# Optimization experiments

Measured on AMD Instinct MI355X. Metric: run time of the kernel, lower is better.

Reference implementation:

```python
import jax, jax.numpy as jnp
import numpy as np

DT = 1.0 / 60.0  # physics timestep
NUM_BODY = 20

# ---- quaternion helpers (xyzw convention, matching the repo) ----

def quat_from_rotvec(rv):
    # rv: [..., 3] axis-angle -> quaternion [..., 4] (x,y,z,w)
    angle = jnp.linalg.norm(rv, axis=-1, keepdims=True)
    half = 0.5 * angle
    safe = jnp.where(angle < 1e-8, 1.0, angle)
    s = jnp.where(angle < 1e-8, 0.5 - angle * angle / 48.0, jnp.sin(half) / safe)
    return jnp.concatenate([rv * s, jnp.cos(half)], axis=-1)


def flip_quat_by_w(q):
    return jnp.where(q[..., 3:4] < 0, -q, q)


def quat_to_vec6d(q):
    # first two columns of the rotation matrix, row-major flattened -> [..., 6]
    x, y, z, w = q[..., 0], q[..., 1], q[..., 2], q[..., 3]
    r00 = 1 - 2 * (y * y + z * z)
    r10 = 2 * (x * y + z * w)
    r20 = 2 * (x * z - y * w)
    r01 = 2 * (x * y - z * w)
    r11 = 1 - 2 * (x * x + z * z)
    r21 = 2 * (y * z + x * w)
    return jnp.stack([r00, r01, r10, r11, r20, r21], axis=-1)


def quat_apply(q, v):
    # rotate v [..., 3] by quaternion q [..., 4]; broadcasts over leading dims
    xyz, w = q[..., :3], q[..., 3:4]
    t = 2.0 * jnp.cross(xyz, v)
    return v + w * t + jnp.cross(xyz, t)


def quat_multiply(p, q):
    pv, pw = p[..., :3], p[..., 3:4]
    qv, qw = q[..., :3], q[..., 3:4]
    v = pw * qv + qw * pv + jnp.cross(pv, qv)
    w = pw * qw - jnp.sum(pv * qv, axis=-1, keepdims=True)
    return jnp.concatenate([v, w], axis=-1)


def quat_integrate(q, omega, dt):
    # q_{t+1} = normalize(q + 0.5*dt * (omega_quat * q))
    omega_q = jnp.concatenate([omega, jnp.zeros_like(omega[..., :1])], axis=-1)
    dq = quat_multiply(omega_q, q)
    r = q + 0.5 * dt * dq
    return r / jnp.linalg.norm(r, axis=-1, keepdims=True)


def integrate_state(state, delta, dt):
    # state: [B, NB, 13] = pos(3) | rot quat(4) | vel(3) | avel(3)
    B, NB, _ = state.shape
    pos, rot = state[..., 0:3], state[..., 3:7]
    vel, avel = state[..., 7:10], state[..., 10:13]
    root_rot = state[:, 0:1, 3:7]                       # [B, 1, 4]
    d3 = delta.reshape(B, -1, 3)                        # [B, 2*NB, 3]
    true_d = quat_apply(root_rot, d3).reshape(B, NB, 6)
    lin, ang = true_d[..., :3], true_d[..., 3:]
    next_vel = vel + lin
    next_avel = avel + ang
    next_pos = pos + next_vel * dt
    next_rot = quat_integrate(rot, next_avel, dt)
    return jnp.concatenate([next_pos, next_rot, next_vel, next_avel], axis=-1)


def setup_inputs() -> dict:
    key = jax.random.key(0)
    ks = jax.random.split(key, 12)
    B = 32768
    inp = {
        "state": jax.random.normal(ks[0], (B, NUM_BODY, 13), jnp.float32),
        "action": jax.random.normal(ks[1], (B, 57), jnp.float32),
        "n_observation": jax.random.normal(ks[2], (B, 300), jnp.float32),
        "W1": jax.random.normal(ks[3], (414, 512), jnp.float32) * 0.05,
        "b1": jax.random.normal(ks[4], (512,), jnp.float32) * 0.05,
        "W2": jax.random.normal(ks[5], (512, 512), jnp.float32) * 0.05,
        "b2": jax.random.normal(ks[6], (512,), jnp.float32) * 0.05,
        "W3": jax.random.normal(ks[7], (512, 120), jnp.float32) * 0.05,
        "b3": jax.random.normal(ks[8], (120,), jnp.float32) * 0.05,
        "delta_mean": jax.random.normal(ks[9], (120,), jnp.float32) * 0.01,
        "delta_std": jax.random.uniform(ks[10], (120,), jnp.float32) + 0.5,
    }
    return inp


def reference(state, action, n_observation, W1, b1, W2, b2, W3, b3, delta_mean, delta_std):
    B = action.shape[0]
    # action rotvecs -> quats -> 6d representation
    aq = flip_quat_by_w(quat_from_rotvec(action.reshape(-1, 3)))
    a6 = quat_to_vec6d(aq).reshape(B, -1)               # [B, 114]
    x = jnp.concatenate([n_observation, a6], axis=-1)   # [B, 414]
    h = jax.nn.relu(x @ W1 + b1)
    h = jax.nn.relu(h @ W2 + b2)
    n_delta = h @ W3 + b3                                # [B, 120]
    delta = n_delta * delta_std + delta_mean             # unnormalize
    return integrate_state(state, delta, DT)
```

## Files before the change

kernel.cpp:

```cpp
#include <hip/hip_runtime.h>
#include <hip/hip_bf16.h>
#include <math.h>

#define DT (1.0f / 60.0f)

typedef __bf16 bf16x8 __attribute__((ext_vector_type(8)));
typedef float f32x4 __attribute__((ext_vector_type(4)));

#define XSTRIDE 848
#define HSTRIDE 1040

struct __attribute__((packed)) f4u {
    float x, y, z, w;
};

__global__ __launch_bounds__(256) void prep_weights(
    const float* __restrict__ W1, const float* __restrict__ W2,
    const float* __restrict__ W3, __hip_bfloat16* __restrict__ W1p,
    __hip_bfloat16* __restrict__ W2p, __hip_bfloat16* __restrict__ W3p) {
    int idx = blockIdx.x * 256 + threadIdx.x;
    if (idx < 212992) {
        int d = idx;
        int e = d & 7, l = (d >> 3) & 63, t = d >> 9;
        int nt = t & 31, ks = t >> 5;
        int n = nt * 16 + (l & 15);
        int k = ks * 32 + (l >> 4) * 8 + e;
        W1p[d] = __float2bfloat16(k < 414 ? W1[k * 512 + n] : 0.0f);
        return;
    }
    idx -= 212992;
    if (idx < 262144) {
        int d = idx;
        int e = d & 7, l = (d >> 3) & 63, t = d >> 9;
        int nt = t & 31, ks = t >> 5;
        int n = nt * 16 + (l & 15);
        int k = ks * 32 + (l >> 4) * 8 + e;
        W2p[d] = __float2bfloat16(W2[k * 512 + n]);
        return;
    }
    idx -= 262144;
    if (idx < 65536) {
        int d = idx;
        int e = d & 7, l = (d >> 3) & 63, t = d >> 9;
        int nt = t & 7, ks = t >> 3;
        int n = nt * 16 + (l & 15);
        int k = ks * 32 + (l >> 4) * 8 + e;
        W3p[d] = __float2bfloat16(n < 120 ? W3[k * 120 + n] : 0.0f);
    }
}

template <int KSTEPS, int NT, int JF, int ASTRIDE>
__device__ __forceinline__ void mlp_layer(const char* Abase, const char* Bbase,
                                          int laneOff, f32x4 (&acc)[4][JF],
                                          bf16x8 (&wpre)[JF]) {
    bf16x8 w0[JF], w1[JF];
#pragma unroll
    for (int j = 0; j < JF; j++) w0[j] = wpre[j];
#pragma unroll 2
    for (int ks = 0; ks < KSTEPS; ks++) {
        if (ks + 1 < KSTEPS) {
            if ((ks & 1) == 0) {
#pragma unroll
                for (int j = 0; j < JF; j++)
                    w1[j] = *(const bf16x8*)(Bbase + (((ks + 1) * NT + j) << 10) + laneOff);
            } else {
#pragma unroll
                for (int j = 0; j < JF; j++)
                    w0[j] = *(const bf16x8*)(Bbase + (((ks + 1) * NT + j) << 10) + laneOff);
            }
        }
        bf16x8 ax[4];
#pragma unroll
        for (int i = 0; i < 4; i++)
            ax[i] = *(const bf16x8*)(Abase + ks * 64 + i * 16 * ASTRIDE);
#pragma unroll
        for (int i = 0; i < 4; i++)
#pragma unroll
            for (int j = 0; j < JF; j++)
                acc[i][j] = __builtin_amdgcn_mfma_f32_16x16x32_bf16(
                    (ks & 1) ? w1[j] : w0[j], ax[i], acc[i][j], 0, 0, 0);
    }
}

__device__ __forceinline__ void store_h_relu_t(const f32x4 (&acc)[4][4],
                                               char* smem, const float* bias,
                                               int wn, int lrow, int kgrp) {
#pragma unroll
    for (int j = 0; j < 4; j++) {
        int f = wn * 64 + j * 16 + kgrp * 4;
        float4 bb = *(const float4*)(bias + f);
#pragma unroll
        for (int i = 0; i < 4; i++) {
            float v0 = acc[i][j][0] + bb.x;
            float v1 = acc[i][j][1] + bb.y;
            float v2 = acc[i][j][2] + bb.z;
            float v3 = acc[i][j][3] + bb.w;
            v0 = v0 > 0.0f ? v0 : 0.0f;
            v1 = v1 > 0.0f ? v1 : 0.0f;
            v2 = v2 > 0.0f ? v2 : 0.0f;
            v3 = v3 > 0.0f ? v3 : 0.0f;
            union { __hip_bfloat162 h2[2]; uint2 u; } pk;
            pk.h2[0] = __float22bfloat162_rn(make_float2(v0, v1));
            pk.h2[1] = __float22bfloat162_rn(make_float2(v2, v3));
            *(uint2*)(smem + (i * 16 + lrow) * HSTRIDE + f * 2) = pk.u;
        }
    }
}

__device__ __forceinline__ void quat_apply3(float qx, float qy, float qz,
                                            float qw, float vx, float vy,
                                            float vz, float& ox, float& oy,
                                            float& oz) {
    float tx = 2.0f * (qy * vz - qz * vy);
    float ty = 2.0f * (qz * vx - qx * vz);
    float tz = 2.0f * (qx * vy - qy * vx);
    ox = vx + qw * tx + (qy * tz - qz * ty);
    oy = vy + qw * ty + (qz * tx - qx * tz);
    oz = vz + qw * tz + (qx * ty - qy * tx);
}

__global__ __launch_bounds__(512, 4) void fused_mlp(
    const float* __restrict__ obs, const float* __restrict__ action,
    const __hip_bfloat16* __restrict__ W1p, const float* __restrict__ b1,
    const __hip_bfloat16* __restrict__ W2p, const float* __restrict__ b2,
    const __hip_bfloat16* __restrict__ W3p, const float* __restrict__ b3,
    const float* __restrict__ dstd, const float* __restrict__ dmean,
    const float* __restrict__ state, float* __restrict__ out) {
    alignas(16) __shared__ char smem[64 * HSTRIDE];
    const int tid = threadIdx.x;
    const int blk = blockIdx.x;
    const int lane = tid & 63, wn = tid >> 6;
    const int lrow = lane & 15, kgrp = lane >> 4;
    const int laneOff = lane * 16;

    bf16x8 wpre[4];
#pragma unroll
    for (int j = 0; j < 4; j++)
        wpre[j] = *(const bf16x8*)((const char*)W1p + (wn << 12) + (j << 10) + laneOff);

    {
        const float4* og = (const float4*)obs + (size_t)blk * 64 * 75;
#pragma unroll
        for (int i = 0; i < 10; i++) {
            int f = tid + i * 512;
            if (f < 4800) {
                int row = f / 75;
                int c4 = f - row * 75;
                float4 v = og[f];
                union { __hip_bfloat162 h2[2]; uint2 u; } pk;
                pk.h2[0] = __float22bfloat162_rn(make_float2(v.x, v.y));
                pk.h2[1] = __float22bfloat162_rn(make_float2(v.z, v.w));
                *(uint2*)(smem + row * XSTRIDE + c4 * 8) = pk.u;
            }
        }
#pragma unroll
        for (int i = 0; i < 3; i++) {
            int q = tid + i * 512;
            if (q < 1216) {
                int row = q / 19;
                int j = q - row * 19;
                const float* a = action + ((size_t)(blk * 64 + row)) * 57 + j * 3;
                float rx = a[0], ry = a[1], rz = a[2];
                float ang = sqrtf(rx * rx + ry * ry + rz * rz);
                float half = 0.5f * ang;
                float s;
                if (ang < 1e-8f)
                    s = 0.5f - ang * ang * (1.0f / 48.0f);
                else
                    s = __sinf(half) / ang;
                float qx = rx * s, qy = ry * s, qz = rz * s, qw = __cosf(half);
                union { __hip_bfloat16 h[6]; uint u[3]; } pq;
                pq.h[0] = __float2bfloat16(1.0f - 2.0f * (qy * qy + qz * qz));
                pq.h[1] = __float2bfloat16(2.0f * (qx * qy - qz * qw));
                pq.h[2] = __float2bfloat16(2.0f * (qx * qy + qz * qw));
                pq.h[3] = __float2bfloat16(1.0f - 2.0f * (qx * qx + qz * qz));
                pq.h[4] = __float2bfloat16(2.0f * (qx * qz - qy * qw));
                pq.h[5] = __float2bfloat16(2.0f * (qy * qz + qx * qw));
                char* p = smem + row * XSTRIDE + 600 + j * 12;
                *(uint*)p = pq.u[0];
                *(uint*)(p + 4) = pq.u[1];
                *(uint*)(p + 8) = pq.u[2];
            }
        }
        if (tid < 320) {
            int row = tid / 5;
            int p = tid - row * 5;
            *(uint*)(smem + row * XSTRIDE + 828 + p * 4) = 0u;
        }
    }
    __syncthreads();

    f32x4 acc[4][4];
    f32x4 zero4 = {0.0f, 0.0f, 0.0f, 0.0f};
#pragma unroll
    for (int i = 0; i < 4; i++)
#pragma unroll
        for (int j = 0; j < 4; j++) acc[i][j] = zero4;

    mlp_layer<13, 32, 4, XSTRIDE>(smem + lrow * XSTRIDE + kgrp * 16,
                                  (const char*)W1p + (wn << 12), laneOff, acc,
                                  wpre);
#pragma unroll
    for (int j = 0; j < 4; j++)
        wpre[j] = *(const bf16x8*)((const char*)W2p + (wn << 12) + (j << 10) + laneOff);
    __syncthreads();
    store_h_relu_t(acc, smem, b1, wn, lrow, kgrp);
    __syncthreads();

#pragma unroll
    for (int i = 0; i < 4; i++)
#pragma unroll
        for (int j = 0; j < 4; j++) acc[i][j] = zero4;
    mlp_layer<16, 32, 4, HSTRIDE>(smem + lrow * HSTRIDE + kgrp * 16,
                                  (const char*)W2p + (wn << 12), laneOff, acc,
                                  wpre);
    const char* Bb3 = (const char*)W3p + (wn << 10);
    bf16x8 c0 = *(const bf16x8*)(Bb3 + laneOff);
    __syncthreads();
    store_h_relu_t(acc, smem, b2, wn, lrow, kgrp);
    __syncthreads();

    f32x4 a3[4];
#pragma unroll
    for (int i = 0; i < 4; i++) a3[i] = zero4;
    {
        const char* Ab = smem + lrow * HSTRIDE + kgrp * 16;
        bf16x8 c1;
#pragma unroll 2
        for (int ks = 0; ks < 16; ks++) {
            if (ks + 1 < 16) {
                if ((ks & 1) == 0)
                    c1 = *(const bf16x8*)(Bb3 + ((ks + 1) << 13) + laneOff);
                else
                    c0 = *(const bf16x8*)(Bb3 + ((ks + 1) << 13) + laneOff);
            }
            bf16x8 ax[4];
#pragma unroll
            for (int i = 0; i < 4; i++)
                ax[i] = *(const bf16x8*)(Ab + ks * 64 + i * 16 * HSTRIDE);
#pragma unroll
            for (int i = 0; i < 4; i++)
                a3[i] = __builtin_amdgcn_mfma_f32_16x16x32_bf16(
                    (ks & 1) ? c1 : c0, ax[i], a3[i], 0, 0, 0);
        }
    }
    __syncthreads();

    float* dl = (float*)smem;
    {
        int f = wn * 16 + kgrp * 4;
        if (f < 120) {
            float4 bb = *(const float4*)(b3 + f);
            float4 sc = *(const float4*)(dstd + f);
            float4 mn = *(const float4*)(dmean + f);
            int bo0 = (f + 0) / 6, o0 = bo0 * 13 + (f + 0) - bo0 * 6;
            int bo1 = (f + 1) / 6, o1 = bo1 * 13 + (f + 1) - bo1 * 6;
            int bo2 = (f + 2) / 6, o2 = bo2 * 13 + (f + 2) - bo2 * 6;
            int bo3 = (f + 3) / 6, o3 = bo3 * 13 + (f + 3) - bo3 * 6;
#pragma unroll
            for (int i = 0; i < 4; i++) {
                float* rs = dl + (i * 16 + lrow) * 260;
                rs[o0] = (a3[i][0] + bb.x) * sc.x + mn.x;
                rs[o1] = (a3[i][1] + bb.y) * sc.y + mn.y;
                rs[o2] = (a3[i][2] + bb.z) * sc.z + mn.z;
                rs[o3] = (a3[i][3] + bb.w) * sc.w + mn.w;
            }
        }
    }
    __syncthreads();

#pragma unroll
    for (int it = 0; it < 3; it++) {
        int idx = tid + it * 512;
        if (idx < 1280) {
            int lr = idx / 20;
            int body = idx - lr * 20;
            const float* sb = state + ((size_t)(blk * 64 + lr)) * 260 + body * 13;
            f4u s0 = *(const f4u*)sb;
            f4u s1 = *(const f4u*)(sb + 4);
            f4u s2 = *(const f4u*)(sb + 8);
            float s12 = sb[12];
            f4u rq = *(const f4u*)(state + ((size_t)(blk * 64 + lr)) * 260 + 3);

            float* slot = dl + lr * 260 + body * 13;
            float d0 = slot[0], d1 = slot[1], d2 = slot[2];
            float d3 = slot[3], d4 = slot[4], d5 = slot[5];

            float lx, ly, lz, ax, ay, az;
            quat_apply3(rq.x, rq.y, rq.z, rq.w, d0, d1, d2, lx, ly, lz);
            quat_apply3(rq.x, rq.y, rq.z, rq.w, d3, d4, d5, ax, ay, az);

            float vx = s1.w + lx, vy = s2.x + ly, vz = s2.y + lz;
            float wx = s2.z + ax, wy = s2.w + ay, wz = s12 + az;
            float px = s0.x + vx * DT, py = s0.y + vy * DT, pz = s0.z + vz * DT;

            float rx = s0.w, ry = s1.x, rz = s1.y, rw = s1.z;
            float dqx = rw * wx + (wy * rz - wz * ry);
            float dqy = rw * wy + (wz * rx - wx * rz);
            float dqz = rw * wz + (wx * ry - wy * rx);
            float dqw = -(wx * rx + wy * ry + wz * rz);
            float h = 0.5f * DT;
            float nx = rx + h * dqx, ny = ry + h * dqy, nz = rz + h * dqz,
                  nw = rw + h * dqw;
            float inv = 1.0f / sqrtf(nx * nx + ny * ny + nz * nz + nw * nw);

            slot[0] = px;
            slot[1] = py;
            slot[2] = pz;
            slot[3] = nx * inv;
            slot[4] = ny * inv;
            slot[5] = nz * inv;
            slot[6] = nw * inv;
            slot[7] = vx;
            slot[8] = vy;
            slot[9] = vz;
            slot[10] = wx;
            slot[11] = wy;
            slot[12] = wz;
        }
    }
    __syncthreads();

    {
        float4* og = (float4*)(out + (size_t)blk * 64 * 260);
#pragma unroll
        for (int i = 0; i < 9; i++) {
            int f = tid + i * 512;
            if (f < 4160) {
                og[f] = *(const float4*)(smem + f * 16);
            }
        }
    }
}

extern "C" void kernel_launch(void* const* d_in, const int* in_sizes, int n_in,
                              void* d_out, int out_size, void* d_ws,
                              size_t ws_size, hipStream_t stream) {
    const float* state = (const float*)d_in[0];
    const float* action = (const float*)d_in[1];
    const float* obs = (const float*)d_in[2];
    const float* W1 = (const float*)d_in[3];
    const float* b1 = (const float*)d_in[4];
    const float* W2 = (const float*)d_in[5];
    const float* b2 = (const float*)d_in[6];
    const float* W3 = (const float*)d_in[7];
    const float* b3 = (const float*)d_in[8];
    const float* dmean = (const float*)d_in[9];
    const float* dstd = (const float*)d_in[10];
    float* out = (float*)d_out;
    char* ws = (char*)d_ws;

    const int B = in_sizes[1] / 57;

    __hip_bfloat16* W1p = (__hip_bfloat16*)(ws);
    __hip_bfloat16* W2p = (__hip_bfloat16*)(ws + 425984);
    __hip_bfloat16* W3p = (__hip_bfloat16*)(ws + 950272);

    prep_weights<<<2112, 256, 0, stream>>>(W1, W2, W3, W1p, W2p, W3p);
    fused_mlp<<<B / 64, 512, 0, stream>>>(obs, action, W1p, b1, W2p, b2, W3p,
                                          b3, dstd, dmean, state, out);
}
```

Baseline: 165.1 us.

## Halve block to four waves, each computing twice the output columns

Switches the fused MLP kernel from 512 threads (8 waves) to 256 threads (4 waves) per block. Each wave now covers 128 output features instead of 64, so it holds a 4x8 accumulator tile and prefetches 8 weight fragments. Every A fragment loaded from shared memory now feeds twice as many MFMAs, which cuts LDS traffic per FLOP. The cost is higher register pressure, fewer waves to hide latency (launch bounds go from 512,4 to 256,2), and more serial work per thread in the load and integration phases.

After: 166.4 us. No clear change (+0.8%).

```diff
diff --git a/kernel.cpp b/kernel.cpp
--- a/kernel.cpp
+++ b/kernel.cpp
@@ -82,12 +82,12 @@
     }
 }
 
-__device__ __forceinline__ void store_h_relu_t(const f32x4 (&acc)[4][4],
+__device__ __forceinline__ void store_h_relu_t(const f32x4 (&acc)[4][8],
                                                char* smem, const float* bias,
                                                int wn, int lrow, int kgrp) {
 #pragma unroll
-    for (int j = 0; j < 4; j++) {
-        int f = wn * 64 + j * 16 + kgrp * 4;
+    for (int j = 0; j < 8; j++) {
+        int f = wn * 128 + j * 16 + kgrp * 4;
         float4 bb = *(const float4*)(bias + f);
 #pragma unroll
         for (int i = 0; i < 4; i++) {
@@ -119,7 +119,7 @@
     oz = vz + qw * tz + (qx * ty - qy * tx);
 }
 
-__global__ __launch_bounds__(512, 4) void fused_mlp(
+__global__ __launch_bounds__(256, 2) void fused_mlp(
     const float* __restrict__ obs, const float* __restrict__ action,
     const __hip_bfloat16* __restrict__ W1p, const float* __restrict__ b1,
     const __hip_bfloat16* __restrict__ W2p, const float* __restrict__ b2,
@@ -133,16 +133,16 @@
     const int lrow = lane & 15, kgrp = lane >> 4;
     const int laneOff = lane * 16;
 
-    bf16x8 wpre[4];
-#pragma unroll
-    for (int j = 0; j < 4; j++)
-        wpre[j] = *(const bf16x8*)((const char*)W1p + (wn << 12) + (j << 10) + laneOff);
+    bf16x8 wpre[8];
+#pragma unroll
+    for (int j = 0; j < 8; j++)
+        wpre[j] = *(const bf16x8*)((const char*)W1p + (wn << 13) + (j << 10) + laneOff);
 
     {
         const float4* og = (const float4*)obs + (size_t)blk * 64 * 75;
 #pragma unroll
-        for (int i = 0; i < 10; i++) {
-            int f = tid + i * 512;
+        for (int i = 0; i < 19; i++) {
+            int f = tid + i * 256;
             if (f < 4800) {
                 int row = f / 75;
                 int c4 = f - row * 75;
@@ -154,8 +154,8 @@
             }
         }
 #pragma unroll
-        for (int i = 0; i < 3; i++) {
-            int q = tid + i * 512;
+        for (int i = 0; i < 5; i++) {
+            int q = tid + i * 256;
             if (q < 1216) {
                 int row = q / 19;
                 int j = q - row * 19;
@@ -182,27 +182,31 @@
                 *(uint*)(p + 8) = pq.u[2];
             }
         }
-        if (tid < 320) {
-            int row = tid / 5;
-            int p = tid - row * 5;
-            *(uint*)(smem + row * XSTRIDE + 828 + p * 4) = 0u;
-        }
-    }
-    __syncthreads();
-
-    f32x4 acc[4][4];
+#pragma unroll
+        for (int i = 0; i < 2; i++) {
+            int id = tid + i * 256;
+            if (id < 320) {
+                int row = id / 5;
+                int p = id - row * 5;
+                *(uint*)(smem + row * XSTRIDE + 828 + p * 4) = 0u;
+            }
+        }
+    }
+    __syncthreads();
+
+    f32x4 acc[4][8];
     f32x4 zero4 = {0.0f, 0.0f, 0.0f, 0.0f};
 #pragma unroll
     for (int i = 0; i < 4; i++)
 #pragma unroll
-        for (int j = 0; j < 4; j++) acc[i][j] = zero4;
-
-    mlp_layer<13, 32, 4, XSTRIDE>(smem + lrow * XSTRIDE + kgrp * 16,
-                                  (const char*)W1p + (wn << 12), laneOff, acc,
+        for (int j = 0; j < 8; j++) acc[i][j] = zero4;
+
+    mlp_layer<13, 32, 8, XSTRIDE>(smem + lrow * XSTRIDE + kgrp * 16,
+                                  (const char*)W1p + (wn << 13), laneOff, acc,
                                   wpre);
 #pragma unroll
-    for (int j = 0; j < 4; j++)
-        wpre[j] = *(const bf16x8*)((const char*)W2p + (wn << 12) + (j << 10) + laneOff);
+    for (int j = 0; j < 8; j++)
+        wpre[j] = *(const bf16x8*)((const char*)W2p + (wn << 13) + (j << 10) + laneOff);
     __syncthreads();
     store_h_relu_t(acc, smem, b1, wn, lrow, kgrp);
     __syncthreads();
@@ -210,29 +214,38 @@
 #pragma unroll
     for (int i = 0; i < 4; i++)
 #pragma unroll
-        for (int j = 0; j < 4; j++) acc[i][j] = zero4;
-    mlp_layer<16, 32, 4, HSTRIDE>(smem + lrow * HSTRIDE + kgrp * 16,
-                                  (const char*)W2p + (wn << 12), laneOff, acc,
+        for (int j = 0; j < 8; j++) acc[i][j] = zero4;
+    mlp_layer<16, 32, 8, HSTRIDE>(smem + lrow * HSTRIDE + kgrp * 16,
+                                  (const char*)W2p + (wn << 13), laneOff, acc,
                                   wpre);
-    const char* Bb3 = (const char*)W3p + (wn << 10);
-    bf16x8 c0 = *(const bf16x8*)(Bb3 + laneOff);
+    const char* Bb3 = (const char*)W3p;
+    bf16x8 c0[2], c1[2];
+#pragma unroll
+    for (int j = 0; j < 2; j++)
+        c0[j] = *(const bf16x8*)(Bb3 + ((wn * 2 + j) << 10) + laneOff);
     __syncthreads();
     store_h_relu_t(acc, smem, b2, wn, lrow, kgrp);
     __syncthreads();
 
-    f32x4 a3[4];
-#pragma unroll
-    for (int i = 0; i < 4; i++) a3[i] = zero4;
+    f32x4 a3[4][2];
+#pragma unroll
+    for (int i = 0; i < 4; i++)
+#pragma unroll
+        for (int j = 0; j < 2; j++) a3[i][j] = zero4;
     {
         const char* Ab = smem + lrow * HSTRIDE + kgrp * 16;
-        bf16x8 c1;
 #pragma unroll 2
         for (int ks = 0; ks < 16; ks++) {
             if (ks + 1 < 16) {
-                if ((ks & 1) == 0)
-                    c1 = *(const bf16x8*)(Bb3 + ((ks + 1) << 13) + laneOff);
-                else
-                    c0 = *(const bf16x8*)(Bb3 + ((ks + 1) << 13) + laneOff);
+                if ((ks & 1) == 0) {
+#pragma unroll
+                    for (int j = 0; j < 2; j++)
+                        c1[j] = *(const bf16x8*)(Bb3 + (((ks + 1) * 8 + wn * 2 + j) << 10) + laneOff);
+                } else {
+#pragma unroll
+                    for (int j = 0; j < 2; j++)
+                        c0[j] = *(const bf16x8*)(Bb3 + (((ks + 1) * 8 + wn * 2 + j) << 10) + laneOff);
+                }
             }
             bf16x8 ax[4];
 #pragma unroll
@@ -240,15 +253,18 @@
                 ax[i] = *(const bf16x8*)(Ab + ks * 64 + i * 16 * HSTRIDE);
 #pragma unroll
             for (int i = 0; i < 4; i++)
-                a3[i] = __builtin_amdgcn_mfma_f32_16x16x32_bf16(
-                    (ks & 1) ? c1 : c0, ax[i], a3[i], 0, 0, 0);
+#pragma unroll
+                for (int j = 0; j < 2; j++)
+                    a3[i][j] = __builtin_amdgcn_mfma_f32_16x16x32_bf16(
+                        (ks & 1) ? c1[j] : c0[j], ax[i], a3[i][j], 0, 0, 0);
         }
     }
     __syncthreads();
 
     float* dl = (float*)smem;
-    {
-        int f = wn * 16 + kgrp * 4;
+#pragma unroll
+    for (int j = 0; j < 2; j++) {
+        int f = wn * 32 + j * 16 + kgrp * 4;
         if (f < 120) {
             float4 bb = *(const float4*)(b3 + f);
             float4 sc = *(const float4*)(dstd + f);
@@ -260,72 +276,70 @@
 #pragma unroll
             for (int i = 0; i < 4; i++) {
                 float* rs = dl + (i * 16 + lrow) * 260;
-                rs[o0] = (a3[i][0] + bb.x) * sc.x + mn.x;
-                rs[o1] = (a3[i][1] + bb.y) * sc.y + mn.y;
-                rs[o2] = (a3[i][2] + bb.z) * sc.z + mn.z;
-                rs[o3] = (a3[i][3] + bb.w) * sc.w + mn.w;
-            }
-        }
-    }
-    __syncthreads();
-
-#pragma unroll
-    for (int it = 0; it < 3; it++) {
-        int idx = tid + it * 512;
-        if (idx < 1280) {
-            int lr = idx / 20;
-            int body = idx - lr * 20;
-            const float* sb = state + ((size_t)(blk * 64 + lr)) * 260 + body * 13;
-            f4u s0 = *(const f4u*)sb;
-            f4u s1 = *(const f4u*)(sb + 4);
-            f4u s2 = *(const f4u*)(sb + 8);
-            float s12 = sb[12];
-            f4u rq = *(const f4u*)(state + ((size_t)(blk * 64 + lr)) * 260 + 3);
-
-            float* slot = dl + lr * 260 + body * 13;
-            float d0 = slot[0], d1 = slot[1], d2 = slot[2];
-            float d3 = slot[3], d4 = slot[4], d5 = slot[5];
-
-            float lx, ly, lz, ax, ay, az;
-            quat_apply3(rq.x, rq.y, rq.z, rq.w, d0, d1, d2, lx, ly, lz);
-            quat_apply3(rq.x, rq.y, rq.z, rq.w, d3, d4, d5, ax, ay, az);
-
-            float vx = s1.w + lx, vy = s2.x + ly, vz = s2.y + lz;
-            float wx = s2.z + ax, wy = s2.w + ay, wz = s12 + az;
-            float px = s0.x + vx * DT, py = s0.y + vy * DT, pz = s0.z + vz * DT;
-
-            float rx = s0.w, ry = s1.x, rz = s1.y, rw = s1.z;
-            float dqx = rw * wx + (wy * rz - wz * ry);
-            float dqy = rw * wy + (wz * rx - wx * rz);
-            float dqz = rw * wz + (wx * ry - wy * rx);
-            float dqw = -(wx * rx + wy * ry + wz * rz);
-            float h = 0.5f * DT;
-            float nx = rx + h * dqx, ny = ry + h * dqy, nz = rz + h * dqz,
-                  nw = rw + h * dqw;
-            float inv = 1.0f / sqrtf(nx * nx + ny * ny + nz * nz + nw * nw);
-
-            slot[0] = px;
-            slot[1] = py;
-            slot[2] = pz;
-            slot[3] = nx * inv;
-            slot[4] = ny * inv;
-            slot[5] = nz * inv;
-            slot[6] = nw * inv;
-            slot[7] = vx;
-            slot[8] = vy;
-            slot[9] = vz;
-            slot[10] = wx;
-            slot[11] = wy;
-            slot[12] = wz;
-        }
+                rs[o0] = (a3[i][j][0] + bb.x) * sc.x + mn.x;
+                rs[o1] = (a3[i][j][1] + bb.y) * sc.y + mn.y;
+                rs[o2] = (a3[i][j][2] + bb.z) * sc.z + mn.z;
+                rs[o3] = (a3[i][j][3] + bb.w) * sc.w + mn.w;
+            }
+        }
+    }
+    __syncthreads();
+
+#pragma unroll
+    for (int it = 0; it < 5; it++) {
+        int idx = tid + it * 256;
+        int lr = idx / 20;
+        int body = idx - lr * 20;
+        const float* sb = state + ((size_t)(blk * 64 + lr)) * 260 + body * 13;
+        f4u s0 = *(const f4u*)sb;
+        f4u s1 = *(const f4u*)(sb + 4);
+        f4u s2 = *(const f4u*)(sb + 8);
+        float s12 = sb[12];
+        f4u rq = *(const f4u*)(state + ((size_t)(blk * 64 + lr)) * 260 + 3);
+
+        float* slot = dl + lr * 260 + body * 13;
+        float d0 = slot[0], d1 = slot[1], d2 = slot[2];
+        float d3 = slot[3], d4 = slot[4], d5 = slot[5];
+
+        float lx, ly, lz, ax, ay, az;
+        quat_apply3(rq.x, rq.y, rq.z, rq.w, d0, d1, d2, lx, ly, lz);
+        quat_apply3(rq.x, rq.y, rq.z, rq.w, d3, d4, d5, ax, ay, az);
+
+        float vx = s1.w + lx, vy = s2.x + ly, vz = s2.y + lz;
+        float wx = s2.z + ax, wy = s2.w + ay, wz = s12 + az;
+        float px = s0.x + vx * DT, py = s0.y + vy * DT, pz = s0.z + vz * DT;
+
+        float rx = s0.w, ry = s1.x, rz = s1.y, rw = s1.z;
+        float dqx = rw * wx + (wy * rz - wz * ry);
+        float dqy = rw * wy + (wz * rx - wx * rz);
+        float dqz = rw * wz + (wx * ry - wy * rx);
+        float dqw = -(wx * rx + wy * ry + wz * rz);
+        float h = 0.5f * DT;
+        float nx = rx + h * dqx, ny = ry + h * dqy, nz = rz + h * dqz,
+              nw = rw + h * dqw;
+        float inv = 1.0f / sqrtf(nx * nx + ny * ny + nz * nz + nw * nw);
+
+        slot[0] = px;
+        slot[1] = py;
+        slot[2] = pz;
+        slot[3] = nx * inv;
+        slot[4] = ny * inv;
+        slot[5] = nz * inv;
+        slot[6] = nw * inv;
+        slot[7] = vx;
+        slot[8] = vy;
+        slot[9] = vz;
+        slot[10] = wx;
+        slot[11] = wy;
+        slot[12] = wz;
     }
     __syncthreads();
 
     {
         float4* og = (float4*)(out + (size_t)blk * 64 * 260);
 #pragma unroll
-        for (int i = 0; i < 9; i++) {
-            int f = tid + i * 512;
+        for (int i = 0; i < 17; i++) {
+            int f = tid + i * 256;
             if (f < 4160) {
                 og[f] = *(const float4*)(smem + f * 16);
             }
@@ -357,6 +371,6 @@
     __hip_bfloat16* W3p = (__hip_bfloat16*)(ws + 950272);
 
     prep_weights<<<2112, 256, 0, stream>>>(W1, W2, W3, W1p, W2p, W3p);
-    fused_mlp<<<B / 64, 512, 0, stream>>>(obs, action, W1p, b1, W2p, b2, W3p,
+    fused_mlp<<<B / 64, 256, 0, stream>>>(obs, action, W1p, b1, W2p, b2, W3p,
                                           b3, dstd, dmean, state, out);
 }
```

## Halve rows per block and double-buffer shared memory to drop barriers

Applied to the files above, without the earlier changes.

Each block now processes 32 batch rows instead of 64, doubling the grid so more blocks run across CUs. Shared memory is split into two slabs that are used in ping-pong fashion, so hidden activations are written to the other slab right after each MMA layer, removing one barrier per layer. The cost is that each block reloads the full weight set for half as many rows, which doubles weight traffic from L2 per output row and lowers MFMA reuse per weight load.

New measurement: 172.3 us. +4.4%, slower.

```diff
diff --git a/kernel.cpp b/kernel.cpp
--- a/kernel.cpp
+++ b/kernel.cpp
@@ -9,6 +9,8 @@
 
 #define XSTRIDE 848
 #define HSTRIDE 1040
+#define ROWS 32
+#define SLAB 33280
 
 struct __attribute__((packed)) f4u {
     float x, y, z, w;
@@ -49,9 +51,9 @@
     }
 }
 
-template <int KSTEPS, int NT, int JF, int ASTRIDE>
+template <int KSTEPS, int NT, int JF, int RT, int ASTRIDE>
 __device__ __forceinline__ void mlp_layer(const char* Abase, const char* Bbase,
-                                          int laneOff, f32x4 (&acc)[4][JF],
+                                          int laneOff, f32x4 (&acc)[RT][JF],
                                           bf16x8 (&wpre)[JF]) {
     bf16x8 w0[JF], w1[JF];
 #pragma unroll
@@ -69,12 +71,12 @@
                     w0[j] = *(const bf16x8*)(Bbase + (((ks + 1) * NT + j) << 10) + laneOff);
             }
         }
-        bf16x8 ax[4];
-#pragma unroll
-        for (int i = 0; i < 4; i++)
+        bf16x8 ax[RT];
+#pragma unroll
+        for (int i = 0; i < RT; i++)
             ax[i] = *(const bf16x8*)(Abase + ks * 64 + i * 16 * ASTRIDE);
 #pragma unroll
-        for (int i = 0; i < 4; i++)
+        for (int i = 0; i < RT; i++)
 #pragma unroll
             for (int j = 0; j < JF; j++)
                 acc[i][j] = __builtin_amdgcn_mfma_f32_16x16x32_bf16(
@@ -82,15 +84,15 @@
     }
 }
 
-__device__ __forceinline__ void store_h_relu_t(const f32x4 (&acc)[4][4],
-                                               char* smem, const float* bias,
+__device__ __forceinline__ void store_h_relu_t(const f32x4 (&acc)[2][4],
+                                               char* dst, const float* bias,
                                                int wn, int lrow, int kgrp) {
 #pragma unroll
     for (int j = 0; j < 4; j++) {
         int f = wn * 64 + j * 16 + kgrp * 4;
         float4 bb = *(const float4*)(bias + f);
 #pragma unroll
-        for (int i = 0; i < 4; i++) {
+        for (int i = 0; i < 2; i++) {
             float v0 = acc[i][j][0] + bb.x;
             float v1 = acc[i][j][1] + bb.y;
             float v2 = acc[i][j][2] + bb.z;
@@ -102,7 +104,7 @@
             union { __hip_bfloat162 h2[2]; uint2 u; } pk;
             pk.h2[0] = __float22bfloat162_rn(make_float2(v0, v1));
             pk.h2[1] = __float22bfloat162_rn(make_float2(v2, v3));
-            *(uint2*)(smem + (i * 16 + lrow) * HSTRIDE + f * 2) = pk.u;
+            *(uint2*)(dst + (i * 16 + lrow) * HSTRIDE + f * 2) = pk.u;
         }
     }
 }
@@ -126,7 +128,9 @@
     const __hip_bfloat16* __restrict__ W3p, const float* __restrict__ b3,
     const float* __restrict__ dstd, const float* __restrict__ dmean,
     const float* __restrict__ state, float* __restrict__ out) {
-    alignas(16) __shared__ char smem[64 * HSTRIDE];
+    alignas(16) __shared__ char smem[2 * SLAB];
+    char* slabA = smem;
+    char* slabB = smem + SLAB;
     const int tid = threadIdx.x;
     const int blk = blockIdx.x;
     const int lane = tid & 63, wn = tid >> 6;
@@ -139,27 +143,27 @@
         wpre[j] = *(const bf16x8*)((const char*)W1p + (wn << 12) + (j << 10) + laneOff);
 
     {
-        const float4* og = (const float4*)obs + (size_t)blk * 64 * 75;
-#pragma unroll
-        for (int i = 0; i < 10; i++) {
+        const float4* og = (const float4*)obs + (size_t)blk * ROWS * 75;
+#pragma unroll
+        for (int i = 0; i < 5; i++) {
             int f = tid + i * 512;
-            if (f < 4800) {
+            if (f < ROWS * 75) {
                 int row = f / 75;
                 int c4 = f - row * 75;
                 float4 v = og[f];
                 union { __hip_bfloat162 h2[2]; uint2 u; } pk;
                 pk.h2[0] = __float22bfloat162_rn(make_float2(v.x, v.y));
                 pk.h2[1] = __float22bfloat162_rn(make_float2(v.z, v.w));
-                *(uint2*)(smem + row * XSTRIDE + c4 * 8) = pk.u;
-            }
-        }
-#pragma unroll
-        for (int i = 0; i < 3; i++) {
+                *(uint2*)(slabA + row * XSTRIDE + c4 * 8) = pk.u;
+            }
+        }
+#pragma unroll
+        for (int i = 0; i < 2; i++) {
             int q = tid + i * 512;
-            if (q < 1216) {
+            if (q < ROWS * 19) {
                 int row = q / 19;
                 int j = q - row * 19;
-                const float* a = action + ((size_t)(blk * 64 + row)) * 57 + j * 3;
+                const float* a = action + ((size_t)(blk * ROWS + row)) * 57 + j * 3;
                 float rx = a[0], ry = a[1], rz = a[2];
                 float ang = sqrtf(rx * rx + ry * ry + rz * rz);
                 float half = 0.5f * ang;
@@ -176,55 +180,53 @@
                 pq.h[3] = __float2bfloat16(1.0f - 2.0f * (qx * qx + qz * qz));
                 pq.h[4] = __float2bfloat16(2.0f * (qx * qz - qy * qw));
                 pq.h[5] = __float2bfloat16(2.0f * (qy * qz + qx * qw));
-                char* p = smem + row * XSTRIDE + 600 + j * 12;
+                char* p = slabA + row * XSTRIDE + 600 + j * 12;
                 *(uint*)p = pq.u[0];
                 *(uint*)(p + 4) = pq.u[1];
                 *(uint*)(p + 8) = pq.u[2];
             }
         }
-        if (tid < 320) {
+        if (tid < ROWS * 5) {
             int row = tid / 5;
             int p = tid - row * 5;
-            *(uint*)(smem + row * XSTRIDE + 828 + p * 4) = 0u;
-        }
-    }
-    __syncthreads();
-
-    f32x4 acc[4][4];
+            *(uint*)(slabA + row * XSTRIDE + 828 + p * 4) = 0u;
+        }
+    }
+    __syncthreads();
+
+    f32x4 acc[2][4];
     f32x4 zero4 = {0.0f, 0.0f, 0.0f, 0.0f};
 #pragma unroll
-    for (int i = 0; i < 4; i++)
+    for (int i = 0; i < 2; i++)
 #pragma unroll
         for (int j = 0; j < 4; j++) acc[i][j] = zero4;
 
-    mlp_layer<13, 32, 4, XSTRIDE>(smem + lrow * XSTRIDE + kgrp * 16,
-                                  (const char*)W1p + (wn << 12), laneOff, acc,
-                                  wpre);
+    mlp_layer<13, 32, 4, 2, XSTRIDE>(slabA + lrow * XSTRIDE + kgrp * 16,
+                                     (const char*)W1p + (wn << 12), laneOff,
+                                     acc, wpre);
+    store_h_relu_t(acc, slabB, b1, wn, lrow, kgrp);
 #pragma unroll
     for (int j = 0; j < 4; j++)
         wpre[j] = *(const bf16x8*)((const char*)W2p + (wn << 12) + (j << 10) + laneOff);
     __syncthreads();
-    store_h_relu_t(acc, smem, b1, wn, lrow, kgrp);
-    __syncthreads();
-
-#pragma unroll
-    for (int i = 0; i < 4; i++)
+
+#pragma unroll
+    for (int i = 0; i < 2; i++)
 #pragma unroll
         for (int j = 0; j < 4; j++) acc[i][j] = zero4;
-    mlp_layer<16, 32, 4, HSTRIDE>(smem + lrow * HSTRIDE + kgrp * 16,
-                                  (const char*)W2p + (wn << 12), laneOff, acc,
-                                  wpre);
+    mlp_layer<16, 32, 4, 2, HSTRIDE>(slabB + lrow * HSTRIDE + kgrp * 16,
+                                     (const char*)W2p + (wn << 12), laneOff,
+                                     acc, wpre);
+    store_h_relu_t(acc, slabA, b2, wn, lrow, kgrp);
     const char* Bb3 = (const char*)W3p + (wn << 10);
     bf16x8 c0 = *(const bf16x8*)(Bb3 + laneOff);
     __syncthreads();
-    store_h_relu_t(acc, smem, b2, wn, lrow, kgrp);
-    __syncthreads();
-
-    f32x4 a3[4];
-#pragma unroll
-    for (int i = 0; i < 4; i++) a3[i] = zero4;
+
+    f32x4 a3[2];
+#pragma unroll
+    for (int i = 0; i < 2; i++) a3[i] = zero4;
     {
-        const char* Ab = smem + lrow * HSTRIDE + kgrp * 16;
+        const char* Ab = slabA + lrow * HSTRIDE + kgrp * 16;
         bf16x8 c1;
 #pragma unroll 2
         for (int ks = 0; ks < 16; ks++) {
@@ -234,19 +236,17 @@
                 else
                     c0 = *(const bf16x8*)(Bb3 + ((ks + 1) << 13) + laneOff);
             }
-            bf16x8 ax[4];
-#pragma unroll
-            for (int i = 0; i < 4; i++)
+            bf16x8 ax[2];
+#pragma unroll
+            for (int i = 0; i < 2; i++)
                 ax[i] = *(const bf16x8*)(Ab + ks * 64 + i * 16 * HSTRIDE);
 #pragma unroll
-            for (int i = 0; i < 4; i++)
+            for (int i = 0; i < 2; i++)
                 a3[i] = __builtin_amdgcn_mfma_f32_16x16x32_bf16(
                     (ks & 1) ? c1 : c0, ax[i], a3[i], 0, 0, 0);
         }
     }
-    __syncthreads();
-
-    float* dl = (float*)smem;
+    float* dl = (float*)slabB;
     {
         int f = wn * 16 + kgrp * 4;
         if (f < 120) {
@@ -258,7 +258,7 @@
             int bo2 = (f + 2) / 6, o2 = bo2 * 13 + (f + 2) - bo2 * 6;
             int bo3 = (f + 3) / 6, o3 = bo3 * 13 + (f + 3) - bo3 * 6;
 #pragma unroll
-            for (int i = 0; i < 4; i++) {
+            for (int i = 0; i < 2; i++) {
                 float* rs = dl + (i * 16 + lrow) * 260;
                 rs[o0] = (a3[i][0] + bb.x) * sc.x + mn.x;
                 rs[o1] = (a3[i][1] + bb.y) * sc.y + mn.y;
@@ -270,17 +270,17 @@
     __syncthreads();
 
 #pragma unroll
-    for (int it = 0; it < 3; it++) {
+    for (int it = 0; it < 2; it++) {
         int idx = tid + it * 512;
-        if (idx < 1280) {
+        if (idx < ROWS * 20) {
             int lr = idx / 20;
             int body = idx - lr * 20;
-            const float* sb = state + ((size_t)(blk * 64 + lr)) * 260 + body * 13;
+            const float* sb = state + ((size_t)(blk * ROWS + lr)) * 260 + body * 13;
             f4u s0 = *(const f4u*)sb;
             f4u s1 = *(const f4u*)(sb + 4);
             f4u s2 = *(const f4u*)(sb + 8);
             float s12 = sb[12];
-            f4u rq = *(const f4u*)(state + ((size_t)(blk * 64 + lr)) * 260 + 3);
+            f4u rq = *(const f4u*)(state + ((size_t)(blk * ROWS + lr)) * 260 + 3);
 
             float* slot = dl + lr * 260 + body * 13;
             float d0 = slot[0], d1 = slot[1], d2 = slot[2];
@@ -322,12 +322,12 @@
     __syncthreads();
 
     {
-        float4* og = (float4*)(out + (size_t)blk * 64 * 260);
-#pragma unroll
-        for (int i = 0; i < 9; i++) {
+        float4* og = (float4*)(out + (size_t)blk * ROWS * 260);
+#pragma unroll
+        for (int i = 0; i < 5; i++) {
             int f = tid + i * 512;
-            if (f < 4160) {
-                og[f] = *(const float4*)(smem + f * 16);
+            if (f < ROWS * 65) {
+                og[f] = *(const float4*)(slabB + f * 16);
             }
         }
     }
@@ -357,6 +357,6 @@
     __hip_bfloat16* W3p = (__hip_bfloat16*)(ws + 950272);
 
     prep_weights<<<2112, 256, 0, stream>>>(W1, W2, W3, W1p, W2p, W3p);
-    fused_mlp<<<B / 64, 512, 0, stream>>>(obs, action, W1p, b1, W2p, b2, W3p,
-                                          b3, dstd, dmean, state, out);
-}
+    fused_mlp<<<B / ROWS, 512, 0, stream>>>(obs, action, W1p, b1, W2p, b2,
+                                            W3p, b3, dstd, dmean, state, out);
+}
```
